# Kernel tuning notes

Hardware: AMD Instinct MI355X
Metric: run time of the kernel (lower is better)

Reference implementation:

```python
import jax, jax.numpy as jnp
import numpy as np

N_NODES = 100000
E = 1600000
IN_C = 128
OUT_C = 128


def setup_inputs() -> dict:
    key = jax.random.key(0)
    k1, k2, k3, k4, k5, k6 = jax.random.split(key, 6)
    x = jax.random.normal(k1, (N_NODES, IN_C), dtype=jnp.float32)
    edge_index = jax.random.randint(k2, (2, E), 0, N_NODES, dtype=jnp.int64)
    s = 1.0 / np.sqrt(IN_C)
    W_src = jax.random.uniform(k3, (OUT_C, IN_C), minval=-s, maxval=s, dtype=jnp.float32)
    b_src = jax.random.uniform(k4, (OUT_C,), minval=-s, maxval=s, dtype=jnp.float32)
    W_dst = jax.random.uniform(k5, (OUT_C, IN_C), minval=-s, maxval=s, dtype=jnp.float32)
    b_dst = jax.random.uniform(k6, (OUT_C,), minval=-s, maxval=s, dtype=jnp.float32)
    return {"x": x, "edge_index": edge_index, "W_src": W_src, "b_src": b_src,
            "W_dst": W_dst, "b_dst": b_dst}


def reference(x, edge_index, W_src, b_src, W_dst, b_dst):
    src, dst = edge_index[0], edge_index[1]
    x_j = x[src]                                             # [E, in]
    agg_sum = jax.ops.segment_sum(x_j, dst, num_segments=x.shape[0])   # [N, in]
    cnt = jax.ops.segment_sum(jnp.ones((src.shape[0],), dtype=x.dtype), dst,
                              num_segments=x.shape[0])       # [N]
    agg_mean = agg_sum / jnp.maximum(cnt, 1.0)[:, None]      # scatter-mean (empty -> 0)
    return agg_mean @ W_src.T + b_src + x @ W_dst.T + b_dst
```

## Files before the change

### kernel.cpp

```cpp
#include <hip/hip_runtime.h>
#include <stdint.h>

typedef __attribute__((ext_vector_type(8))) short short8;
typedef __attribute__((ext_vector_type(4))) float floatx4;
typedef __attribute__((ext_vector_type(4))) int intx4;
typedef __attribute__((ext_vector_type(2))) int intx2;
typedef __attribute__((ext_vector_type(2))) float floatx2;

#define NN 100000
#define NE 1600000
#define NB_SCAN 196
#define HIST_BLKS 6250
#define CONV_BLKS 6250
#define NODES_PER_G 12500
#define CAP 64

#define NBKT 196
#define TILE 4096
#define BIN_BLKS 391
#define CAPB 8704

__device__ __forceinline__ short f2bf(float f) {
  unsigned u = __builtin_bit_cast(unsigned, f);
  u = (u + 0x7fffu + ((u >> 16) & 1u)) >> 16;
  return (short)u;
}
__device__ __forceinline__ float bf2f(unsigned hi16) {
  return __builtin_bit_cast(float, hi16 << 16);
}

#define BK_GC_B 0
#define BK_GBUF_B 4096
#define BK_SLOT_B 14000000
#define BK_ROW_B 21000000
#define BK_DEG_B 21500000
#define BK_XB_B 22000000
#define BK_XQ_B 47600000
#define BK_WB_B 60400000
#define BK_NEED 60465536ull

#define WS_DEG 0
#define WS_ROW 100000
#define WS_CUR 200000
#define WS_BSUM 300000
#define WS_BOFF 300256
#define WS_SLOT 300512
#define WS_XB_BYTE 7602048


__global__ __launch_bounds__(256) void bin_conv_k(const int* __restrict__ ei,
                                                  int* __restrict__ gcount,
                                                  int2* __restrict__ gbuf,
                                                  const float* __restrict__ x,
                                                  short* __restrict__ xb,
                                                  int* __restrict__ xq,
                                                  const float* __restrict__ Wsrc,
                                                  const float* __restrict__ Wdst,
                                                  short* __restrict__ wb) {
  const int blk = blockIdx.x;
  if (blk < BIN_BLKS) {
    __shared__ int ls[TILE], ld[TILE];
    __shared__ int hcnt[NBKT], hbase[NBKT], hcur[NBKT], gposs[NBKT];
    __shared__ int sc[256];
    __shared__ int ntot;
    const int tid = threadIdx.x;
    const int tile = blk * TILE;

    int s_[16], d_[16];
#pragma unroll
    for (int k = 0; k < 16; ++k) {
      const int e = tile + tid + k * 256;
      if (e < NE) {
        s_[k] = ei[e];
        d_[k] = ei[NE + e];
      } else {
        s_[k] = 0; d_[k] = -1;
      }
    }
    if (tid < NBKT) hcnt[tid] = 0;
    __syncthreads();
#pragma unroll
    for (int k = 0; k < 16; ++k)
      if (d_[k] >= 0) atomicAdd(&hcnt[d_[k] >> 9], 1);
    __syncthreads();
    sc[tid] = (tid < NBKT) ? hcnt[tid] : 0;
    __syncthreads();
    for (int off = 1; off < 256; off <<= 1) {
      const int v = (tid >= off) ? sc[tid - off] : 0;
      __syncthreads();
      sc[tid] += v;
      __syncthreads();
    }
    if (tid < NBKT) {
      hbase[tid] = sc[tid] - hcnt[tid];
      gposs[tid] = atomicAdd(&gcount[tid], hcnt[tid]);
      hcur[tid] = 0;
    }
    if (tid == 0) ntot = sc[NBKT - 1];
    __syncthreads();
#pragma unroll
    for (int k = 0; k < 16; ++k) {
      if (d_[k] >= 0) {
        const int b = d_[k] >> 9;
        const int r = hbase[b] + atomicAdd(&hcur[b], 1);
        ls[r] = s_[k];
        ld[r] = d_[k];
      }
    }
    __syncthreads();
    const int nt = ntot;
    for (int i = tid; i < nt; i += 256) {
      const int d = ld[i];
      const int b = d >> 9;
      const int pos = gposs[b] + (i - hbase[b]);
      if (pos < CAPB) {
        int2 e; e.x = ls[i]; e.y = d;
        gbuf[(size_t)b * CAPB + pos] = e;
      }
    }
  } else if (blk < BIN_BLKS + CONV_BLKS) {
    const int t = (blk - BIN_BLKS) * 256 + threadIdx.x;
    const floatx4* x4 = reinterpret_cast<const floatx4*>(x);
    floatx4 f0 = __builtin_nontemporal_load(&x4[2 * t]);
    floatx4 f1 = __builtin_nontemporal_load(&x4[2 * t + 1]);
    short8 v;
    v[0] = f2bf(f0.x); v[1] = f2bf(f0.y); v[2] = f2bf(f0.z); v[3] = f2bf(f0.w);
    v[4] = f2bf(f1.x); v[5] = f2bf(f1.y); v[6] = f2bf(f1.z); v[7] = f2bf(f1.w);
    reinterpret_cast<short8*>(xb)[t] = v;
    int w0 = __builtin_amdgcn_cvt_pk_fp8_f32(f0.x, f0.y, 0, false);
    w0 = __builtin_amdgcn_cvt_pk_fp8_f32(f0.z, f0.w, w0, true);
    int w1 = __builtin_amdgcn_cvt_pk_fp8_f32(f1.x, f1.y, 0, false);
    w1 = __builtin_amdgcn_cvt_pk_fp8_f32(f1.z, f1.w, w1, true);
    intx2 q; q.x = w0; q.y = w1;
    reinterpret_cast<intx2*>(xq)[t] = q;
  } else {
    const int t = threadIdx.x;
#pragma unroll
    for (int m = 0; m < 2; ++m) {
      const float* W = m ? Wdst : Wsrc;
      short8* dst = reinterpret_cast<short8*>(wb + m * 16384);
#pragma unroll
      for (int c = 0; c < 8; ++c) {
        const int i8 = t * 8 + c;
        floatx4 f0 = reinterpret_cast<const floatx4*>(W)[2 * i8];
        floatx4 f1 = reinterpret_cast<const floatx4*>(W)[2 * i8 + 1];
        short8 v;
        v[0] = f2bf(f0.x); v[1] = f2bf(f0.y); v[2] = f2bf(f0.z); v[3] = f2bf(f0.w);
        v[4] = f2bf(f1.x); v[5] = f2bf(f1.y); v[6] = f2bf(f1.z); v[7] = f2bf(f1.w);
        dst[i8] = v;
      }
    }
  }
}

__global__ __launch_bounds__(512) void bucket_csr_k(const int* __restrict__ gcount,
                                                    const int2* __restrict__ gbuf,
                                                    int* __restrict__ slotg,
                                                    int* __restrict__ rowstg,
                                                    int* __restrict__ degg) {
  __shared__ int cnt[512], sc[512], cur[512];
  __shared__ int lslot[CAPB];
  const int b = blockIdx.x;
  const int tid = threadIdx.x;
  const int nb = min(gcount[b], CAPB);
  const size_t base = (size_t)b * CAPB;

  cnt[tid] = 0;
  __syncthreads();
  for (int i = tid; i < nb; i += 512)
    atomicAdd(&cnt[gbuf[base + i].y & 511], 1);
  __syncthreads();
  sc[tid] = cnt[tid];
  __syncthreads();
  for (int off = 1; off < 512; off <<= 1) {
    const int v = (tid >= off) ? sc[tid - off] : 0;
    __syncthreads();
    sc[tid] += v;
    __syncthreads();
  }
  const int rst = sc[tid] - cnt[tid];
  cur[tid] = rst;
  __syncthreads();
  for (int i = tid; i < nb; i += 512) {
    const int2 e = gbuf[base + i];
    const int p = atomicAdd(&cur[e.y & 511], 1);
    lslot[p] = e.x << 6;
  }
  __syncthreads();
  for (int i = tid; i < nb; i += 512) slotg[base + i] = lslot[i];
  const int n = b * 512 + tid;
  if (n < NN) {
    rowstg[n] = (int)base + rst;
    degg[n] = cnt[tid];
  }
}

__global__ __launch_bounds__(256) void gather_csr_k(const unsigned short* __restrict__ xq,
                                                    const int* __restrict__ rowstg,
                                                    const int* __restrict__ degg,
                                                    const int* __restrict__ slotg,
                                                    float* __restrict__ out) {
  const int lane = threadIdx.x & 63;
  const int w = (blockIdx.x * 256 + threadIdx.x) >> 6;
  if (w >= NN) return;
  const int st = rowstg[w];
  const int dg = degg[w];
  float2 acc = {0.f, 0.f};
  for (int b0 = 0; b0 < dg; b0 += 64) {
    const int nbk = min(64, dg - b0);
    const int idx = (lane < nbk) ? slotg[st + b0 + lane] : 0;
    int i = 0;
    for (; i + 4 <= nbk; i += 4) {
      const int s0 = __shfl(idx, i), s1 = __shfl(idx, i + 1);
      const int s2 = __shfl(idx, i + 2), s3 = __shfl(idx, i + 3);
      const int v0 = xq[s0 + lane];
      const int v1 = xq[s1 + lane];
      const int v2 = xq[s2 + lane];
      const int v3 = xq[s3 + lane];
      floatx2 p0 = __builtin_amdgcn_cvt_pk_f32_fp8(v0, false);
      floatx2 p1 = __builtin_amdgcn_cvt_pk_f32_fp8(v1, false);
      floatx2 p2 = __builtin_amdgcn_cvt_pk_f32_fp8(v2, false);
      floatx2 p3 = __builtin_amdgcn_cvt_pk_f32_fp8(v3, false);
      acc.x += p0.x; acc.y += p0.y;
      acc.x += p1.x; acc.y += p1.y;
      acc.x += p2.x; acc.y += p2.y;
      acc.x += p3.x; acc.y += p3.y;
    }
    for (; i < nbk; ++i) {
      const int s = __shfl(idx, i);
      const int v = xq[s + lane];
      floatx2 p = __builtin_amdgcn_cvt_pk_f32_fp8(v, false);
      acc.x += p.x; acc.y += p.y;
    }
  }
  const float inv = 1.0f / fmaxf((float)dg, 1.0f);
  const unsigned b0w = (unsigned)(unsigned short)f2bf(acc.x * inv);
  const unsigned b1w = (unsigned)(unsigned short)f2bf(acc.y * inv);
  reinterpret_cast<unsigned*>(out + (size_t)w * 128 + 64)[lane] = b0w | (b1w << 16);
}

__global__ __launch_bounds__(512) void sage_gemm_k(
    const short* __restrict__ xb, const short* __restrict__ wb,
    const float* __restrict__ bsrc, const float* __restrict__ bdst,
    float* __restrict__ out) {
  __shared__ short Blds[128 * 128];
  char* const Bb = reinterpret_cast<char*>(Blds);
  const int tid = threadIdx.x;
  const int n0 = blockIdx.x * 128;
  const int wid = tid >> 6;
  const int lane = tid & 63;
  const int r0 = wid * 16;
  const int lrow = lane & 15;
  const int kh = (lane >> 4) * 8;
  const int arow = r0 + lrow;
  const int n = n0 + arow;
  const bool valid = (n < NN);

  floatx4 acc[8];
  floatx4 zero = {0.f, 0.f, 0.f, 0.f};
#pragma unroll
  for (int f = 0; f < 8; ++f) acc[f] = zero;

#pragma unroll
  for (int h = 0; h < 2; ++h) {
    {
      const int j = tid >> 2;
      const int q = tid & 3;
      const short8* src8 = reinterpret_cast<const short8*>(
          wb + h * 16384 + j * 128 + q * 32);
      const int sw = (j & 7) << 4;
      const int base = j * 256 + q * 64;
#pragma unroll
      for (int c = 0; c < 4; ++c)
        *reinterpret_cast<short8*>(Bb + ((base + c * 16) ^ sw)) = src8[c];
    }
    __syncthreads();

    const short* arow_ptr = (h == 0)
        ? reinterpret_cast<const short*>(out + (size_t)n * 128 + 64)
        : (xb + (size_t)n * 128);
    short8 a[4];
#pragma unroll
    for (int ks = 0; ks < 4; ++ks) {
      if (valid)
        a[ks] = *reinterpret_cast<const short8*>(arow_ptr + ks * 32 + kh);
      else
        a[ks] = short8{};
    }
#pragma unroll
    for (int ks = 0; ks < 4; ++ks) {
      const int kb = (ks * 32 + kh) * 2;
#pragma unroll
      for (int f = 0; f < 8; ++f) {
        const int j = f * 16 + lrow;
        short8 b = *reinterpret_cast<const short8*>(
            Bb + ((j * 256 + kb) ^ ((j & 7) << 4)));
        acc[f] = __builtin_amdgcn_mfma_f32_16x16x32_bf16(a[ks], b, acc[f], 0, 0, 0);
      }
    }
    __syncthreads();
  }

  const int crow = r0 + (lane >> 4) * 4;
#pragma unroll
  for (int f = 0; f < 8; ++f) {
    const int j = f * 16 + lrow;
    const float bias = bsrc[j] + bdst[j];
#pragma unroll
    for (int rg = 0; rg < 4; ++rg) {
      const int nn = n0 + crow + rg;
      if (nn < NN) out[(size_t)nn * 128 + j] = acc[f][rg] + bias;
    }
  }
}


__global__ __launch_bounds__(256) void hist_conv_k(const int* __restrict__ ei,
                                                   int* __restrict__ deg,
                                                   const float* __restrict__ x,
                                                   short* __restrict__ xb) {
  const int b = blockIdx.x;
  if (b < HIST_BLKS) {
    int e = b * 256 + threadIdx.x;
    if (e < NE) atomicAdd(&deg[ei[NE + e]], 1);
  } else {
    const int t = (b - HIST_BLKS) * 256 + threadIdx.x;
    const float4* x4 = reinterpret_cast<const float4*>(x);
    float4 f0 = x4[2 * t];
    float4 f1 = x4[2 * t + 1];
    short8 v;
    v[0] = f2bf(f0.x); v[1] = f2bf(f0.y); v[2] = f2bf(f0.z); v[3] = f2bf(f0.w);
    v[4] = f2bf(f1.x); v[5] = f2bf(f1.y); v[6] = f2bf(f1.z); v[7] = f2bf(f1.w);
    reinterpret_cast<short8*>(xb)[t] = v;
  }
}

__global__ __launch_bounds__(256) void scan1_k(const int* __restrict__ deg,
                                               int* __restrict__ bsum) {
  __shared__ int s[256];
  const int t = threadIdx.x;
  const int i0 = blockIdx.x * 512 + 2 * t;
  int v = 0;
  if (i0 < NN) v += deg[i0];
  if (i0 + 1 < NN) v += deg[i0 + 1];
  s[t] = v;
  __syncthreads();
  for (int off = 128; off > 0; off >>= 1) {
    if (t < off) s[t] += s[t + off];
    __syncthreads();
  }
  if (t == 0) bsum[blockIdx.x] = s[0];
}

__global__ __launch_bounds__(256) void scan2_k(const int* __restrict__ bsum,
                                               int* __restrict__ boff) {
  __shared__ int s[256];
  const int t = threadIdx.x;
  const int v = (t < NB_SCAN) ? bsum[t] : 0;
  s[t] = v;
  __syncthreads();
  for (int off = 1; off < 256; off <<= 1) {
    int a = (t >= off) ? s[t - off] : 0;
    __syncthreads();
    s[t] += a;
    __syncthreads();
  }
  if (t < NB_SCAN) boff[t] = s[t] - v;
}

__global__ __launch_bounds__(256) void scan3_k(const int* __restrict__ deg,
                                               const int* __restrict__ boff,
                                               int* __restrict__ rowst,
                                               int* __restrict__ cursor) {
  __shared__ int s[256];
  const int t = threadIdx.x;
  const int i0 = blockIdx.x * 512 + 2 * t;
  const int v0 = (i0 < NN) ? deg[i0] : 0;
  const int v1 = (i0 + 1 < NN) ? deg[i0 + 1] : 0;
  const int tsum = v0 + v1;
  s[t] = tsum;
  __syncthreads();
  for (int off = 1; off < 256; off <<= 1) {
    int a = (t >= off) ? s[t - off] : 0;
    __syncthreads();
    s[t] += a;
    __syncthreads();
  }
  const int excl = s[t] - tsum + boff[blockIdx.x];
  if (i0 < NN) { rowst[i0] = excl; cursor[i0] = excl; }
  if (i0 + 1 < NN) { rowst[i0 + 1] = excl + v0; cursor[i0 + 1] = excl + v0; }
}

__global__ __launch_bounds__(256) void fill_k(const int* __restrict__ ei,
                                              int* __restrict__ cursor,
                                              int* __restrict__ slot) {
  const int g = blockIdx.x & 7;
  const int lo = g * NODES_PER_G;
  const int hi = lo + NODES_PER_G;
  const int stride = (gridDim.x >> 3) * 256;
  for (int e = (blockIdx.x >> 3) * 256 + threadIdx.x; e < NE; e += stride) {
    const int d = ei[NE + e];
    if (d >= lo && d < hi) {
      const int p = atomicAdd(&cursor[d], 1);
      slot[p] = ei[e];
    }
  }
}

__global__ __launch_bounds__(256) void gather_bf_k(const short* __restrict__ xb,
                                                   const int* __restrict__ rowst,
                                                   const int* __restrict__ deg,
                                                   const int* __restrict__ slot,
                                                   float* __restrict__ out) {
  const int lane = threadIdx.x & 63;
  const int w = (blockIdx.x * 256 + threadIdx.x) >> 6;
  if (w >= NN) return;
  const int st = rowst[w];
  const int dg = deg[w];
  const unsigned* xu = reinterpret_cast<const unsigned*>(xb);
  float2 acc = {0.f, 0.f};
  for (int b0 = 0; b0 < dg; b0 += 64) {
    const int nb = min(64, dg - b0);
    const int idx = (lane < nb) ? slot[st + b0 + lane] : 0;
    for (int i = 0; i < nb; ++i) {
      const int s = __shfl(idx, i);
      unsigned u = xu[(size_t)s * 64 + lane];
      acc.x += bf2f(u & 0xffffu); acc.y += bf2f(u >> 16);
    }
  }
  const float inv = 1.0f / fmaxf((float)dg, 1.0f);
  const unsigned b0w = (unsigned)(unsigned short)f2bf(acc.x * inv);
  const unsigned b1w = (unsigned)(unsigned short)f2bf(acc.y * inv);
  reinterpret_cast<unsigned*>(out + (size_t)w * 128 + 64)[lane] = b0w | (b1w << 16);
}

__global__ __launch_bounds__(512) void sage_gemm_fb_k(
    const short* __restrict__ xb,
    const float* __restrict__ Wsrc, const float* __restrict__ bsrc,
    const float* __restrict__ Wdst, const float* __restrict__ bdst,
    float* __restrict__ out) {
  __shared__ short Alds[128 * 128];
  __shared__ short Blds[128 * 128];
  const int tid = threadIdx.x;
  const int n0 = blockIdx.x * 128;

  const int wid = tid >> 6;
  const int lane = tid & 63;
  const int r0 = wid * 16;
  const int lrow = lane & 15;
  const int kh = (lane >> 4) * 8;
  const int arow = r0 + lrow;
  const int asw = (arow & 7) << 4;

  floatx4 acc[8];
  floatx4 zero = {0.f, 0.f, 0.f, 0.f};
#pragma unroll
  for (int f = 0; f < 8; ++f) acc[f] = zero;

#pragma unroll
  for (int h = 0; h < 2; ++h) {
    {
      const int j = tid >> 2;
      const int q = tid & 3;
      const float* src = ((h == 0) ? Wsrc : Wdst) + j * 128 + q * 32;
      const int sw = (j & 7) << 4;
      const int base = j * 256 + q * 64;
#pragma unroll
      for (int c = 0; c < 4; ++c) {
        float4 f0 = reinterpret_cast<const float4*>(src)[2 * c];
        float4 f1 = reinterpret_cast<const float4*>(src)[2 * c + 1];
        short8 v;
        v[0] = f2bf(f0.x); v[1] = f2bf(f0.y); v[2] = f2bf(f0.z); v[3] = f2bf(f0.w);
        v[4] = f2bf(f1.x); v[5] = f2bf(f1.y); v[6] = f2bf(f1.z); v[7] = f2bf(f1.w);
        *reinterpret_cast<short8*>(reinterpret_cast<char*>(Blds) + ((base + c * 16) ^ sw)) = v;
      }
    }
    {
      const int r = tid >> 2;
      const int q = tid & 3;
      const int n = n0 + r;
      const int sw = (r & 7) << 4;
      const int base = r * 256 + q * 64;
      if (n < NN) {
        const char* srcb = (h == 0)
            ? (reinterpret_cast<const char*>(out + (size_t)n * 128 + 64) + q * 64)
            : (reinterpret_cast<const char*>(xb + (size_t)n * 128) + q * 64);
#pragma unroll
        for (int c = 0; c < 4; ++c) {
          short8 v = *reinterpret_cast<const short8*>(srcb + c * 16);
          *reinterpret_cast<short8*>(reinterpret_cast<char*>(Alds) + ((base + c * 16) ^ sw)) = v;
        }
      } else {
        short8 z = {};
#pragma unroll
        for (int c = 0; c < 4; ++c)
          *reinterpret_cast<short8*>(reinterpret_cast<char*>(Alds) + ((base + c * 16) ^ sw)) = z;
      }
    }
    __syncthreads();

#pragma unroll
    for (int ks = 0; ks < 4; ++ks) {
      const int kb = (ks * 32 + kh) * 2;
      short8 a = *reinterpret_cast<const short8*>(
          reinterpret_cast<const char*>(Alds) + ((arow * 256 + kb) ^ asw));
#pragma unroll
      for (int f = 0; f < 8; ++f) {
        const int j = f * 16 + lrow;
        short8 b = *reinterpret_cast<const short8*>(
            reinterpret_cast<const char*>(Blds) + ((j * 256 + kb) ^ ((j & 7) << 4)));
        acc[f] = __builtin_amdgcn_mfma_f32_16x16x32_bf16(a, b, acc[f], 0, 0, 0);
      }
    }
    __syncthreads();
  }

  const int crow = r0 + (lane >> 4) * 4;
#pragma unroll
  for (int f = 0; f < 8; ++f) {
    const int j = f * 16 + lrow;
    const float bias = bsrc[j] + bdst[j];
#pragma unroll
    for (int rg = 0; rg < 4; ++rg) {
      const int n = n0 + crow + rg;
      if (n < NN) out[(size_t)n * 128 + j] = acc[f][rg] + bias;
    }
  }
}

extern "C" void kernel_launch(void* const* d_in, const int* in_sizes, int n_in,
                              void* d_out, int out_size, void* d_ws, size_t ws_size,
                              hipStream_t stream) {
  const float* x = (const float*)d_in[0];
  const int* ei = (const int*)d_in[1];
  const float* Wsrc = (const float*)d_in[2];
  const float* bsrc = (const float*)d_in[3];
  const float* Wdst = (const float*)d_in[4];
  const float* bdst = (const float*)d_in[5];
  float* out = (float*)d_out;

  if (ws_size >= BK_NEED) {
    int* gcount = (int*)((char*)d_ws + BK_GC_B);
    int2* gbuf = (int2*)((char*)d_ws + BK_GBUF_B);
    int* slotg = (int*)((char*)d_ws + BK_SLOT_B);
    int* rowstg = (int*)((char*)d_ws + BK_ROW_B);
    int* degg = (int*)((char*)d_ws + BK_DEG_B);
    short* xb = (short*)((char*)d_ws + BK_XB_B);
    int* xq = (int*)((char*)d_ws + BK_XQ_B);
    short* wb = (short*)((char*)d_ws + BK_WB_B);
    hipMemsetAsync(gcount, 0, NBKT * sizeof(int), stream);
    bin_conv_k<<<BIN_BLKS + CONV_BLKS + 1, 256, 0, stream>>>(
        ei, gcount, gbuf, x, xb, xq, Wsrc, Wdst, wb);
    bucket_csr_k<<<NBKT, 512, 0, stream>>>(gcount, gbuf, slotg, rowstg, degg);
    gather_csr_k<<<(NN * 64 + 255) / 256, 256, 0, stream>>>(
        (const unsigned short*)xq, rowstg, degg, slotg, out);
    sage_gemm_k<<<(NN + 127) / 128, 512, 0, stream>>>(xb, wb, bsrc, bdst, out);
    return;
  }

  int* ws = (int*)d_ws;
  int* deg = ws + WS_DEG;
  int* rowst = ws + WS_ROW;
  int* cursor = ws + WS_CUR;
  int* bsum = ws + WS_BSUM;
  int* boff = ws + WS_BOFF;
  int* slot = ws + WS_SLOT;
  short* xb = (short*)((char*)d_ws + WS_XB_BYTE);

  hipMemsetAsync(deg, 0, NN * sizeof(int), stream);
  hist_conv_k<<<HIST_BLKS + CONV_BLKS, 256, 0, stream>>>(ei, deg, x, xb);
  scan1_k<<<NB_SCAN, 256, 0, stream>>>(deg, bsum);
  scan2_k<<<1, 256, 0, stream>>>(bsum, boff);
  scan3_k<<<NB_SCAN, 256, 0, stream>>>(deg, boff, rowst, cursor);
  fill_k<<<1024, 256, 0, stream>>>(ei, cursor, slot);
  gather_bf_k<<<(NN * 64 + 255) / 256, 256, 0, stream>>>(xb, rowst, deg, slot, out);
  sage_gemm_fb_k<<<(NN + 127) / 128, 512, 0, stream>>>(xb, Wsrc, bsrc, Wdst, bdst, out);
}
```

Measured before the change: 125.5 us.

## Pack binned edges into single int and gather two neighbors per wave with dword loads

The binning pass now stores each edge as one 32-bit word (source shifted by 9 bits, low 9 bits of destination), halving gbuf traffic between bin_conv_k and bucket_csr_k. The gather kernel splits the wave into two 32-lane halves, each loading a 4-byte fp8 group per lane from a different neighbor row, then combines the halves with a cross-half shuffle. This aims to cut the number of load instructions per edge and widen each memory access. Slot offsets switch to dword units to match. The packing relies on source ids fitting in 23 bits.

```diff
diff --git a/kernel.cpp b/kernel.cpp
--- a/kernel.cpp
+++ b/kernel.cpp
@@ -50,7 +50,7 @@
 
 __global__ __launch_bounds__(256) void bin_conv_k(const int* __restrict__ ei,
                                                   int* __restrict__ gcount,
-                                                  int2* __restrict__ gbuf,
+                                                  int* __restrict__ gbuf,
                                                   const float* __restrict__ x,
                                                   short* __restrict__ xb,
                                                   int* __restrict__ xq,
@@ -113,10 +113,8 @@
       const int d = ld[i];
       const int b = d >> 9;
       const int pos = gposs[b] + (i - hbase[b]);
-      if (pos < CAPB) {
-        int2 e; e.x = ls[i]; e.y = d;
-        gbuf[(size_t)b * CAPB + pos] = e;
-      }
+      if (pos < CAPB)
+        gbuf[(size_t)b * CAPB + pos] = (ls[i] << 9) | (d & 511);
     }
   } else if (blk < BIN_BLKS + CONV_BLKS) {
     const int t = (blk - BIN_BLKS) * 256 + threadIdx.x;
@@ -154,7 +152,7 @@
 }
 
 __global__ __launch_bounds__(512) void bucket_csr_k(const int* __restrict__ gcount,
-                                                    const int2* __restrict__ gbuf,
+                                                    const int* __restrict__ gbuf,
                                                     int* __restrict__ slotg,
                                                     int* __restrict__ rowstg,
                                                     int* __restrict__ degg) {
@@ -168,7 +166,7 @@
   cnt[tid] = 0;
   __syncthreads();
   for (int i = tid; i < nb; i += 512)
-    atomicAdd(&cnt[gbuf[base + i].y & 511], 1);
+    atomicAdd(&cnt[gbuf[base + i] & 511], 1);
   __syncthreads();
   sc[tid] = cnt[tid];
   __syncthreads();
@@ -182,9 +180,9 @@
   cur[tid] = rst;
   __syncthreads();
   for (int i = tid; i < nb; i += 512) {
-    const int2 e = gbuf[base + i];
-    const int p = atomicAdd(&cur[e.y & 511], 1);
-    lslot[p] = e.x << 6;
+    const int pk = gbuf[base + i];
+    const int p = atomicAdd(&cur[pk & 511], 1);
+    lslot[p] = (pk >> 9) << 5;
   }
   __syncthreads();
   for (int i = tid; i < nb; i += 512) slotg[base + i] = lslot[i];
@@ -195,7 +193,7 @@
   }
 }
 
-__global__ __launch_bounds__(256) void gather_csr_k(const unsigned short* __restrict__ xq,
+__global__ __launch_bounds__(256) void gather_csr_k(const unsigned* __restrict__ xqu,
                                                     const int* __restrict__ rowstg,
                                                     const int* __restrict__ degg,
                                                     const int* __restrict__ slotg,
@@ -205,38 +203,67 @@
   if (w >= NN) return;
   const int st = rowstg[w];
   const int dg = degg[w];
-  float2 acc = {0.f, 0.f};
+  const int half = lane >> 5;
+  const int col = lane & 31;
+  floatx4 acc = {0.f, 0.f, 0.f, 0.f};
+
   for (int b0 = 0; b0 < dg; b0 += 64) {
     const int nbk = min(64, dg - b0);
     const int idx = (lane < nbk) ? slotg[st + b0 + lane] : 0;
     int i = 0;
-    for (; i + 4 <= nbk; i += 4) {
-      const int s0 = __shfl(idx, i), s1 = __shfl(idx, i + 1);
-      const int s2 = __shfl(idx, i + 2), s3 = __shfl(idx, i + 3);
-      const int v0 = xq[s0 + lane];
-      const int v1 = xq[s1 + lane];
-      const int v2 = xq[s2 + lane];
-      const int v3 = xq[s3 + lane];
-      floatx2 p0 = __builtin_amdgcn_cvt_pk_f32_fp8(v0, false);
-      floatx2 p1 = __builtin_amdgcn_cvt_pk_f32_fp8(v1, false);
-      floatx2 p2 = __builtin_amdgcn_cvt_pk_f32_fp8(v2, false);
-      floatx2 p3 = __builtin_amdgcn_cvt_pk_f32_fp8(v3, false);
-      acc.x += p0.x; acc.y += p0.y;
-      acc.x += p1.x; acc.y += p1.y;
-      acc.x += p2.x; acc.y += p2.y;
-      acc.x += p3.x; acc.y += p3.y;
-    }
-    for (; i < nbk; ++i) {
+    for (; i + 8 <= nbk; i += 8) {
+      const int s0 = __shfl(idx, i + half);
+      const int s1 = __shfl(idx, i + 2 + half);
+      const int s2 = __shfl(idx, i + 4 + half);
+      const int s3 = __shfl(idx, i + 6 + half);
+      const unsigned v0 = xqu[s0 + col];
+      const unsigned v1 = xqu[s1 + col];
+      const unsigned v2 = xqu[s2 + col];
+      const unsigned v3 = xqu[s3 + col];
+      floatx2 l0 = __builtin_amdgcn_cvt_pk_f32_fp8(v0, false);
+      floatx2 h0 = __builtin_amdgcn_cvt_pk_f32_fp8(v0, true);
+      floatx2 l1 = __builtin_amdgcn_cvt_pk_f32_fp8(v1, false);
+      floatx2 h1 = __builtin_amdgcn_cvt_pk_f32_fp8(v1, true);
+      floatx2 l2 = __builtin_amdgcn_cvt_pk_f32_fp8(v2, false);
+      floatx2 h2 = __builtin_amdgcn_cvt_pk_f32_fp8(v2, true);
+      floatx2 l3 = __builtin_amdgcn_cvt_pk_f32_fp8(v3, false);
+      floatx2 h3 = __builtin_amdgcn_cvt_pk_f32_fp8(v3, true);
+      acc.x += l0.x + l1.x + l2.x + l3.x;
+      acc.y += l0.y + l1.y + l2.y + l3.y;
+      acc.z += h0.x + h1.x + h2.x + h3.x;
+      acc.w += h0.y + h1.y + h2.y + h3.y;
+    }
+    for (; i + 2 <= nbk; i += 2) {
+      const int s = __shfl(idx, i + half);
+      const unsigned v = xqu[s + col];
+      floatx2 lo = __builtin_amdgcn_cvt_pk_f32_fp8(v, false);
+      floatx2 hi = __builtin_amdgcn_cvt_pk_f32_fp8(v, true);
+      acc.x += lo.x; acc.y += lo.y; acc.z += hi.x; acc.w += hi.y;
+    }
+    if (i < nbk) {
       const int s = __shfl(idx, i);
-      const int v = xq[s + lane];
-      floatx2 p = __builtin_amdgcn_cvt_pk_f32_fp8(v, false);
-      acc.x += p.x; acc.y += p.y;
-    }
-  }
-  const float inv = 1.0f / fmaxf((float)dg, 1.0f);
-  const unsigned b0w = (unsigned)(unsigned short)f2bf(acc.x * inv);
-  const unsigned b1w = (unsigned)(unsigned short)f2bf(acc.y * inv);
-  reinterpret_cast<unsigned*>(out + (size_t)w * 128 + 64)[lane] = b0w | (b1w << 16);
+      if (half == 0) {
+        const unsigned v = xqu[s + col];
+        floatx2 lo = __builtin_amdgcn_cvt_pk_f32_fp8(v, false);
+        floatx2 hi = __builtin_amdgcn_cvt_pk_f32_fp8(v, true);
+        acc.x += lo.x; acc.y += lo.y; acc.z += hi.x; acc.w += hi.y;
+      }
+    }
+  }
+  acc.x += __shfl_xor(acc.x, 32);
+  acc.y += __shfl_xor(acc.y, 32);
+  acc.z += __shfl_xor(acc.z, 32);
+  acc.w += __shfl_xor(acc.w, 32);
+  if (half == 0) {
+    const float inv = 1.0f / fmaxf((float)dg, 1.0f);
+    intx2 r;
+    r.x = (int)(((unsigned)(unsigned short)f2bf(acc.x * inv)) |
+                ((unsigned)(unsigned short)f2bf(acc.y * inv) << 16));
+    r.y = (int)(((unsigned)(unsigned short)f2bf(acc.z * inv)) |
+                ((unsigned)(unsigned short)f2bf(acc.w * inv) << 16));
+    *reinterpret_cast<intx2*>(
+        reinterpret_cast<char*>(out + (size_t)w * 128 + 64) + col * 8) = r;
+  }
 }
 
 __global__ __launch_bounds__(512) void sage_gemm_k(
@@ -541,7 +568,7 @@
 
   if (ws_size >= BK_NEED) {
     int* gcount = (int*)((char*)d_ws + BK_GC_B);
-    int2* gbuf = (int2*)((char*)d_ws + BK_GBUF_B);
+    int* gbuf = (int*)((char*)d_ws + BK_GBUF_B);
     int* slotg = (int*)((char*)d_ws + BK_SLOT_B);
     int* rowstg = (int*)((char*)d_ws + BK_ROW_B);
     int* degg = (int*)((char*)d_ws + BK_DEG_B);
@@ -553,7 +580,7 @@
         ei, gcount, gbuf, x, xb, xq, Wsrc, Wdst, wb);
     bucket_csr_k<<<NBKT, 512, 0, stream>>>(gcount, gbuf, slotg, rowstg, degg);
     gather_csr_k<<<(NN * 64 + 255) / 256, 256, 0, stream>>>(
-        (const unsigned short*)xq, rowstg, degg, slotg, out);
+        (const unsigned*)xq, rowstg, degg, slotg, out);
     sage_gemm_k<<<(NN + 127) / 128, 512, 0, stream>>>(xb, wb, bsrc, bdst, out);
     return;
   }
```

Measured after the change: 119.9 us, median of 2. 4.4% less time.

## Pack binned edges into one int and gather four edges per wave with 8-byte loads

Applied to the files above, without the earlier changes.

The binned edge buffer now stores source and low destination bits packed into a single 32-bit word instead of an int2, which halves the intermediate write and read traffic between binning and CSR build. The gather kernel splits each wave into four 16-lane groups that each read 8 fp8 values per lane with one 8-byte load, so four neighbor rows are processed per step. It then reduces across the groups with shuffles and writes 16-byte stores from one group. The packing relies on source indices fitting in 23 bits, and the final cross-group shuffle reduction adds some overhead per node.

```diff
diff --git a/kernel.cpp b/kernel.cpp
--- a/kernel.cpp
+++ b/kernel.cpp
@@ -50,7 +50,7 @@
 
 __global__ __launch_bounds__(256) void bin_conv_k(const int* __restrict__ ei,
                                                   int* __restrict__ gcount,
-                                                  int2* __restrict__ gbuf,
+                                                  int* __restrict__ gbuf,
                                                   const float* __restrict__ x,
                                                   short* __restrict__ xb,
                                                   int* __restrict__ xq,
@@ -113,10 +113,8 @@
       const int d = ld[i];
       const int b = d >> 9;
       const int pos = gposs[b] + (i - hbase[b]);
-      if (pos < CAPB) {
-        int2 e; e.x = ls[i]; e.y = d;
-        gbuf[(size_t)b * CAPB + pos] = e;
-      }
+      if (pos < CAPB)
+        gbuf[(size_t)b * CAPB + pos] = (ls[i] << 9) | (d & 511);
     }
   } else if (blk < BIN_BLKS + CONV_BLKS) {
     const int t = (blk - BIN_BLKS) * 256 + threadIdx.x;
@@ -154,7 +152,7 @@
 }
 
 __global__ __launch_bounds__(512) void bucket_csr_k(const int* __restrict__ gcount,
-                                                    const int2* __restrict__ gbuf,
+                                                    const int* __restrict__ gbuf,
                                                     int* __restrict__ slotg,
                                                     int* __restrict__ rowstg,
                                                     int* __restrict__ degg) {
@@ -168,7 +166,7 @@
   cnt[tid] = 0;
   __syncthreads();
   for (int i = tid; i < nb; i += 512)
-    atomicAdd(&cnt[gbuf[base + i].y & 511], 1);
+    atomicAdd(&cnt[gbuf[base + i] & 511], 1);
   __syncthreads();
   sc[tid] = cnt[tid];
   __syncthreads();
@@ -182,9 +180,9 @@
   cur[tid] = rst;
   __syncthreads();
   for (int i = tid; i < nb; i += 512) {
-    const int2 e = gbuf[base + i];
-    const int p = atomicAdd(&cur[e.y & 511], 1);
-    lslot[p] = e.x << 6;
+    const int pk = gbuf[base + i];
+    const int p = atomicAdd(&cur[pk & 511], 1);
+    lslot[p] = (pk >> 9) << 5;
   }
   __syncthreads();
   for (int i = tid; i < nb; i += 512) slotg[base + i] = lslot[i];
@@ -195,7 +193,7 @@
   }
 }
 
-__global__ __launch_bounds__(256) void gather_csr_k(const unsigned short* __restrict__ xq,
+__global__ __launch_bounds__(256) void gather_csr_k(const unsigned* __restrict__ xqu,
                                                     const int* __restrict__ rowstg,
                                                     const int* __restrict__ degg,
                                                     const int* __restrict__ slotg,
@@ -205,38 +203,53 @@
   if (w >= NN) return;
   const int st = rowstg[w];
   const int dg = degg[w];
-  float2 acc = {0.f, 0.f};
+  const int q = lane >> 4;
+  const int col = lane & 15;
+  floatx4 accA = {0.f, 0.f, 0.f, 0.f};
+  floatx4 accB = {0.f, 0.f, 0.f, 0.f};
+
   for (int b0 = 0; b0 < dg; b0 += 64) {
     const int nbk = min(64, dg - b0);
-    const int idx = (lane < nbk) ? slotg[st + b0 + lane] : 0;
-    int i = 0;
-    for (; i + 4 <= nbk; i += 4) {
-      const int s0 = __shfl(idx, i), s1 = __shfl(idx, i + 1);
-      const int s2 = __shfl(idx, i + 2), s3 = __shfl(idx, i + 3);
-      const int v0 = xq[s0 + lane];
-      const int v1 = xq[s1 + lane];
-      const int v2 = xq[s2 + lane];
-      const int v3 = xq[s3 + lane];
-      floatx2 p0 = __builtin_amdgcn_cvt_pk_f32_fp8(v0, false);
-      floatx2 p1 = __builtin_amdgcn_cvt_pk_f32_fp8(v1, false);
-      floatx2 p2 = __builtin_amdgcn_cvt_pk_f32_fp8(v2, false);
-      floatx2 p3 = __builtin_amdgcn_cvt_pk_f32_fp8(v3, false);
-      acc.x += p0.x; acc.y += p0.y;
-      acc.x += p1.x; acc.y += p1.y;
-      acc.x += p2.x; acc.y += p2.y;
-      acc.x += p3.x; acc.y += p3.y;
-    }
-    for (; i < nbk; ++i) {
-      const int s = __shfl(idx, i);
-      const int v = xq[s + lane];
-      floatx2 p = __builtin_amdgcn_cvt_pk_f32_fp8(v, false);
-      acc.x += p.x; acc.y += p.y;
-    }
-  }
-  const float inv = 1.0f / fmaxf((float)dg, 1.0f);
-  const unsigned b0w = (unsigned)(unsigned short)f2bf(acc.x * inv);
-  const unsigned b1w = (unsigned)(unsigned short)f2bf(acc.y * inv);
-  reinterpret_cast<unsigned*>(out + (size_t)w * 128 + 64)[lane] = b0w | (b1w << 16);
+    const int idx = (lane < nbk)
+        ? __builtin_nontemporal_load(&slotg[st + b0 + lane]) : 0;
+#pragma unroll 4
+    for (int i = 0; i < nbk; i += 4) {
+      const int j = i + q;
+      const int s = __shfl(idx, j & 63);
+      if (j < nbk) {
+        const intx2 v = *reinterpret_cast<const intx2*>(xqu + s + col * 2);
+        floatx2 l0 = __builtin_amdgcn_cvt_pk_f32_fp8(v.x, false);
+        floatx2 h0 = __builtin_amdgcn_cvt_pk_f32_fp8(v.x, true);
+        floatx2 l1 = __builtin_amdgcn_cvt_pk_f32_fp8(v.y, false);
+        floatx2 h1 = __builtin_amdgcn_cvt_pk_f32_fp8(v.y, true);
+        accA.x += l0.x; accA.y += l0.y; accA.z += h0.x; accA.w += h0.y;
+        accB.x += l1.x; accB.y += l1.y; accB.z += h1.x; accB.w += h1.y;
+      }
+    }
+  }
+  accA.x += __shfl_xor(accA.x, 16); accA.x += __shfl_xor(accA.x, 32);
+  accA.y += __shfl_xor(accA.y, 16); accA.y += __shfl_xor(accA.y, 32);
+  accA.z += __shfl_xor(accA.z, 16); accA.z += __shfl_xor(accA.z, 32);
+  accA.w += __shfl_xor(accA.w, 16); accA.w += __shfl_xor(accA.w, 32);
+  accB.x += __shfl_xor(accB.x, 16); accB.x += __shfl_xor(accB.x, 32);
+  accB.y += __shfl_xor(accB.y, 16); accB.y += __shfl_xor(accB.y, 32);
+  accB.z += __shfl_xor(accB.z, 16); accB.z += __shfl_xor(accB.z, 32);
+  accB.w += __shfl_xor(accB.w, 16); accB.w += __shfl_xor(accB.w, 32);
+
+  if (q == 0) {
+    const float inv = 1.0f / fmaxf((float)dg, 1.0f);
+    intx4 r;
+    r.x = (int)(((unsigned)(unsigned short)f2bf(accA.x * inv)) |
+                ((unsigned)(unsigned short)f2bf(accA.y * inv) << 16));
+    r.y = (int)(((unsigned)(unsigned short)f2bf(accA.z * inv)) |
+                ((unsigned)(unsigned short)f2bf(accA.w * inv) << 16));
+    r.z = (int)(((unsigned)(unsigned short)f2bf(accB.x * inv)) |
+                ((unsigned)(unsigned short)f2bf(accB.y * inv) << 16));
+    r.w = (int)(((unsigned)(unsigned short)f2bf(accB.z * inv)) |
+                ((unsigned)(unsigned short)f2bf(accB.w * inv) << 16));
+    *reinterpret_cast<intx4*>(
+        reinterpret_cast<char*>(out + (size_t)w * 128 + 64) + col * 16) = r;
+  }
 }
 
 __global__ __launch_bounds__(512) void sage_gemm_k(
@@ -541,7 +554,7 @@
 
   if (ws_size >= BK_NEED) {
     int* gcount = (int*)((char*)d_ws + BK_GC_B);
-    int2* gbuf = (int2*)((char*)d_ws + BK_GBUF_B);
+    int* gbuf = (int*)((char*)d_ws + BK_GBUF_B);
     int* slotg = (int*)((char*)d_ws + BK_SLOT_B);
     int* rowstg = (int*)((char*)d_ws + BK_ROW_B);
     int* degg = (int*)((char*)d_ws + BK_DEG_B);
@@ -553,7 +566,7 @@
         ei, gcount, gbuf, x, xb, xq, Wsrc, Wdst, wb);
     bucket_csr_k<<<NBKT, 512, 0, stream>>>(gcount, gbuf, slotg, rowstg, degg);
     gather_csr_k<<<(NN * 64 + 255) / 256, 256, 0, stream>>>(
-        (const unsigned short*)xq, rowstg, degg, slotg, out);
+        (const unsigned*)xq, rowstg, degg, slotg, out);
     sage_gemm_k<<<(NN + 127) / 128, 512, 0, stream>>>(xb, wb, bsrc, bdst, out);
     return;
   }
```

Result: no change. 128.0 us (+2.0%).
